# Kernel tuning notes

Hardware: AMD Instinct MI355X
Metric: run time of the kernel (lower is better)

Reference implementation:

```python
import jax, jax.numpy as jnp
import numpy as np

N_NODES = 100000
N_EDGES = 1600000
IN_FEATS = 256
OUT_FEATS = 128


def setup_inputs() -> dict:
    key = jax.random.key(0)
    k1, k2, k3, k4 = jax.random.split(key, 4)
    feat = jax.random.normal(k1, (N_NODES, IN_FEATS), dtype=jnp.float32)
    src = jax.random.randint(k2, (N_EDGES,), 0, N_NODES, dtype=jnp.int64)
    dst = jax.random.randint(k3, (N_EDGES,), 0, N_NODES, dtype=jnp.int64)
    W = jax.random.normal(k4, (IN_FEATS, OUT_FEATS), dtype=jnp.float32) * (1.0 / np.sqrt(IN_FEATS))
    b = jnp.zeros((OUT_FEATS,), dtype=jnp.float32)
    return {"feat": feat, "src": src, "dst": dst, "W": W, "b": b}


def reference(feat, src, dst, W, b):
    # norm = 'both': symmetric degree normalization, clip degrees at 1
    ones = jnp.ones((src.shape[0],), dtype=jnp.float32)
    out_deg = jax.ops.segment_sum(ones, src, num_segments=N_NODES)  # out-degree per src node
    in_deg = jax.ops.segment_sum(ones, dst, num_segments=N_NODES)   # in-degree per dst node
    norm_src = jnp.power(jnp.clip(out_deg, 1.0, None), -0.5)[:, None]  # (N,1)
    norm_dst = jnp.power(jnp.clip(in_deg, 1.0, None), -0.5)[:, None]   # (N,1)

    h = feat * norm_src
    # in_feats (256) > out_feats (128): apply W before aggregation
    h = h @ W  # (N, out_feats)
    # copy_src + sum aggregation over edges (SpMM)
    msgs = h[src]  # (E, out_feats)
    rst = jax.ops.segment_sum(msgs, dst, num_segments=N_NODES)  # (N, out_feats)
    rst = rst * norm_dst
    rst = rst + b
    return rst
```

## Files before the change

### kernel.cpp

```cpp
#include <hip/hip_runtime.h>
#include <hip/hip_bf16.h>
#include <cstddef>

#define NN 100000
#define NE 1600000
#define INF 256
#define OUTF 128
#define NBKT 196
#define BSH 9
#define P1B 250
#define EPB 6400
#define SCL (NBKT * P1B)
#define SCLP 49152

typedef __bf16 bf16x8 __attribute__((ext_vector_type(8)));
typedef float f32x4 __attribute__((ext_vector_type(4)));

__device__ __forceinline__ float bflo(uint v) { return __uint_as_float(v << 16); }
__device__ __forceinline__ float bfhi(uint v) { return __uint_as_float(v & 0xffff0000u); }

__device__ __forceinline__ void gload16(const void* g, void* l) {
  __builtin_amdgcn_global_load_lds((const __attribute__((address_space(1))) void*)g,
                                   (__attribute__((address_space(3))) void*)l, 16, 0, 0);
}

__global__ __launch_bounds__(256) void k_p1a(const int* __restrict__ src,
                                             const int* __restrict__ dst,
                                             int* __restrict__ ghd,
                                             int* __restrict__ ghs,
                                             const float* __restrict__ W,
                                             __bf16* __restrict__ Wt) {
  if (blockIdx.x >= P1B) {
    int i = (blockIdx.x - P1B) * 256 + threadIdx.x;
    if (i < SCLP - SCL) { ghd[SCL + i] = 0; ghs[SCL + i] = 0; }
    int n = i & 127, k = i >> 7;
    Wt[n * INF + k] = (__bf16)W[k * OUTF + n];
    return;
  }
  __shared__ int lhd[NBKT], lhs[NBKT];
  const int t = threadIdx.x;
  if (t < NBKT) { lhd[t] = 0; lhs[t] = 0; }
  __syncthreads();
  const int base = blockIdx.x * EPB;
#pragma unroll
  for (int i = 0; i < EPB / 256; ++i) {
    int e = base + i * 256 + t;
    atomicAdd(&lhd[dst[e] >> BSH], 1);
    atomicAdd(&lhs[src[e] >> BSH], 1);
  }
  __syncthreads();
  if (t < NBKT) {
    ghd[t * P1B + blockIdx.x] = lhd[t];
    ghs[t * P1B + blockIdx.x] = lhs[t];
  }
}

__global__ __launch_bounds__(1024) void k_p1b(int* __restrict__ ghd,
                                              int* __restrict__ ghs,
                                              int* __restrict__ row_start) {
  int* a = blockIdx.x ? ghs : ghd;
  __shared__ int wsum[16];
  const int t = threadIdx.x;
  const int lane = t & 63, wid = t >> 6;
  int4 v[12];
  const int4* p = (const int4*)(a + t * 48);
#pragma unroll
  for (int i = 0; i < 12; ++i) v[i] = p[i];
  int s = 0;
#pragma unroll
  for (int i = 0; i < 12; ++i) s += v[i].x + v[i].y + v[i].z + v[i].w;
  const int mysum = s;
#pragma unroll
  for (int d = 1; d < 64; d <<= 1) {
    int u = __shfl_up(s, d);
    if (lane >= d) s += u;
  }
  if (lane == 63) wsum[wid] = s;
  __syncthreads();
  if (wid == 0) {
    int ws = (lane < 16) ? wsum[lane] : 0;
    int inc = ws;
#pragma unroll
    for (int d = 1; d < 16; d <<= 1) {
      int u = __shfl_up(inc, d);
      if (lane >= d) inc += u;
    }
    if (lane < 16) wsum[lane] = inc - ws;
  }
  __syncthreads();
  int ex = wsum[wid] + s - mysum;
#pragma unroll
  for (int i = 0; i < 12; ++i) {
    int4 w;
    w.x = ex; ex += v[i].x;
    w.y = ex; ex += v[i].y;
    w.z = ex; ex += v[i].z;
    w.w = ex; ex += v[i].w;
    ((int4*)(a + t * 48))[i] = w;
  }
  if (blockIdx.x == 0 && t == 0) row_start[NN] = NE;
}

__global__ __launch_bounds__(256) void k_p1c(const int* __restrict__ src,
                                             const int* __restrict__ dst,
                                             const int* __restrict__ ghd,
                                             const int* __restrict__ ghs,
                                             uint* __restrict__ rec_d,
                                             ushort* __restrict__ rec_s) {
  __shared__ int od[NBKT], os[NBKT];
  const int t = threadIdx.x;
  if (t < NBKT) {
    od[t] = ghd[t * P1B + blockIdx.x];
    os[t] = ghs[t * P1B + blockIdx.x];
  }
  __syncthreads();
  const int base = blockIdx.x * EPB;
#pragma unroll
  for (int i = 0; i < EPB / 256; ++i) {
    int e = base + i * 256 + t;
    int s = src[e], d = dst[e];
    int p = atomicAdd(&od[d >> BSH], 1);
    rec_d[p] = ((uint)s << BSH) | (uint)(d & 511);
    int q = atomicAdd(&os[s >> BSH], 1);
    rec_s[q] = (ushort)(s & 511);
  }
}

__global__ __launch_bounds__(256) void k_p2(const int* __restrict__ ghd,
                                            const int* __restrict__ ghs,
                                            const uint* __restrict__ rec_d,
                                            const ushort* __restrict__ rec_s,
                                            int* __restrict__ edge_src,
                                            int* __restrict__ row_start,
                                            float* __restrict__ ns) {
  __shared__ int lh[512];
  __shared__ int sc[256];
  const int k = blockIdx.x, t = threadIdx.x;
  {
    const int base = ghd[k * P1B];
    const int end = (k == NBKT - 1) ? NE : ghd[(k + 1) * P1B];
    lh[t] = 0; lh[t + 256] = 0;
    __syncthreads();
    for (int j = base + t; j < end; j += 256) atomicAdd(&lh[rec_d[j] & 511], 1);
    __syncthreads();
    int a0 = lh[2 * t], a1 = lh[2 * t + 1];
    sc[t] = a0 + a1;
    __syncthreads();
    for (int off = 1; off < 256; off <<= 1) {
      int add = (t >= off) ? sc[t - off] : 0;
      __syncthreads();
      sc[t] += add;
      __syncthreads();
    }
    int ex = t ? sc[t - 1] : 0;
    int e0 = ex, e1 = ex + a0;
    int n0 = k * 512 + 2 * t;
    if (n0 < NN) row_start[n0] = base + e0;
    if (n0 + 1 < NN) row_start[n0 + 1] = base + e1;
    __syncthreads();
    lh[2 * t] = base + e0;
    lh[2 * t + 1] = base + e1;
    __syncthreads();
    for (int j = base + t; j < end; j += 256) {
      uint r = rec_d[j];
      int p = atomicAdd(&lh[r & 511], 1);
      edge_src[p] = (int)(r >> BSH);
    }
  }
  __syncthreads();
  {
    const int base = ghs[k * P1B];
    const int end = (k == NBKT - 1) ? NE : ghs[(k + 1) * P1B];
    lh[t] = 0; lh[t + 256] = 0;
    __syncthreads();
    for (int j = base + t; j < end; j += 256) atomicAdd(&lh[rec_s[j]], 1);
    __syncthreads();
    int n0 = k * 512 + t, n1 = n0 + 256;
    if (n0 < NN) { int c = lh[t];       ns[n0] = rsqrtf((float)(c > 1 ? c : 1)); }
    if (n1 < NN) { int c = lh[t + 256]; ns[n1] = rsqrtf((float)(c > 1 ? c : 1)); }
  }
}

__global__ __launch_bounds__(256, 2) void k_gemm(const float* __restrict__ feat,
                                                 const __bf16* __restrict__ Wt,
                                                 __bf16* __restrict__ h) {
  __shared__ float lA[2][128 * 64];
  const int tid = threadIdx.x;
  const int w = tid >> 6, l = tid & 63;
  const int lr = l & 15, lg = l >> 4;
  const int bm = blockIdx.x * 128;

#define STAGE(b, t)                                                            \
  {                                                                            \
    _Pragma("unroll")                                                          \
    for (int i = 0; i < 8; ++i) {                                              \
      int chunk = i * 256 + tid;                                               \
      int row = chunk >> 4, cp = chunk & 15;                                   \
      int gr = bm + row; if (gr >= NN) gr = NN - 1;                            \
      int sc = cp ^ (row & 7);                                                 \
      gload16(feat + (size_t)gr * INF + (t) * 64 + sc * 4,                     \
              &lA[b][0] + (size_t)chunk * 4);                                  \
    }                                                                          \
  }

  STAGE(0, 0);

  f32x4 acc[2][8];
#pragma unroll
  for (int i = 0; i < 2; ++i)
#pragma unroll
    for (int j = 0; j < 8; ++j) acc[i][j] = (f32x4)0.0f;

  __syncthreads();

  for (int t = 0; t < 4; ++t) {
    if (t < 3) STAGE((t + 1) & 1, t + 1);
    const float* lb = &lA[t & 1][0];
    const __bf16* bp = Wt + (size_t)lr * INF + t * 64 + lg * 8;
    bf16x8 bfrag[2][8];
#pragma unroll
    for (int kk = 0; kk < 2; ++kk)
#pragma unroll
      for (int nf = 0; nf < 8; ++nf)
        bfrag[kk][nf] = *(const bf16x8*)(bp + (size_t)nf * 16 * INF + kk * 32);
#pragma unroll
    for (int kk = 0; kk < 2; ++kk) {
#pragma unroll
      for (int mf = 0; mf < 2; ++mf) {
        int row = w * 32 + mf * 16 + lr;
        int c = kk * 8 + lg * 2;
        f32x4 x0 = *(const f32x4*)(lb + row * 64 + ((c ^ (row & 7)) << 2));
        f32x4 x1 = *(const f32x4*)(lb + row * 64 + (((c + 1) ^ (row & 7)) << 2));
        bf16x8 a;
#pragma unroll
        for (int j = 0; j < 4; ++j) {
          a[j] = (__bf16)x0[j];
          a[4 + j] = (__bf16)x1[j];
        }
#pragma unroll
        for (int nf = 0; nf < 8; ++nf)
          acc[mf][nf] = __builtin_amdgcn_mfma_f32_16x16x32_bf16(a, bfrag[kk][nf], acc[mf][nf], 0, 0, 0);
      }
    }
    __syncthreads();
  }

#pragma unroll
  for (int mf = 0; mf < 2; ++mf) {
#pragma unroll
    for (int r = 0; r < 4; ++r) {
      int row = bm + w * 32 + mf * 16 + lg * 4 + r;
      if (row < NN) {
        __bf16* hp = h + (size_t)row * OUTF + lr;
#pragma unroll
        for (int nf = 0; nf < 8; ++nf)
          hp[nf * 16] = (__bf16)(acc[mf][nf][r]);
      }
    }
  }
#undef STAGE
}

__global__ __launch_bounds__(256) void k_aggr(const uint4* __restrict__ h4,
                                              const int* __restrict__ row_start,
                                              const float* __restrict__ ns,
                                              const int* __restrict__ edge_src,
                                              const float* __restrict__ bias,
                                              float* __restrict__ out) {
  const int wave = threadIdx.x >> 6;
  const int lane = threadIdx.x & 63;
  const int q = lane >> 4;
  const int cl = lane & 15;
  const int n = blockIdx.x * 4 + wave;
  const int s0 = row_start[n];
  const int s1 = row_start[n + 1];
  const int cnt = s1 - s0;

  float a0 = 0.f, a1 = 0.f, a2 = 0.f, a3 = 0.f, a4 = 0.f, a5 = 0.f, a6 = 0.f, a7 = 0.f;
  for (int j0 = 0; j0 < cnt; j0 += 64) {
    int nb = cnt - j0; if (nb > 64) nb = 64;
    int idv = 0; float nsv = 0.f;
    if (lane < nb) idv = edge_src[s0 + j0 + lane];
    if (lane < nb) nsv = ns[idv];
#pragma unroll 4
    for (int j = 0; j < nb; j += 4) {
      int jj = j + q;
      int e = __shfl(idv, jj);
      float w = __shfl(nsv, jj);
      if (jj < nb) {
        uint4 v = h4[(size_t)e * 16 + cl];
        a0 += w * bflo(v.x); a1 += w * bfhi(v.x);
        a2 += w * bflo(v.y); a3 += w * bfhi(v.y);
        a4 += w * bflo(v.z); a5 += w * bfhi(v.z);
        a6 += w * bflo(v.w); a7 += w * bfhi(v.w);
      }
    }
  }
  a0 += __shfl_xor(a0, 16); a1 += __shfl_xor(a1, 16); a2 += __shfl_xor(a2, 16); a3 += __shfl_xor(a3, 16);
  a4 += __shfl_xor(a4, 16); a5 += __shfl_xor(a5, 16); a6 += __shfl_xor(a6, 16); a7 += __shfl_xor(a7, 16);
  a0 += __shfl_xor(a0, 32); a1 += __shfl_xor(a1, 32); a2 += __shfl_xor(a2, 32); a3 += __shfl_xor(a3, 32);
  a4 += __shfl_xor(a4, 32); a5 += __shfl_xor(a5, 32); a6 += __shfl_xor(a6, 32); a7 += __shfl_xor(a7, 32);

  if (q == 0) {
    float ndv = rsqrtf((float)(cnt > 1 ? cnt : 1));
    const float4* b4 = (const float4*)bias;
    float4 ba = b4[2 * cl], bb = b4[2 * cl + 1];
    float4 o0, o1;
    o0.x = a0 * ndv + ba.x; o0.y = a1 * ndv + ba.y; o0.z = a2 * ndv + ba.z; o0.w = a3 * ndv + ba.w;
    o1.x = a4 * ndv + bb.x; o1.y = a5 * ndv + bb.y; o1.z = a6 * ndv + bb.z; o1.w = a7 * ndv + bb.w;
    float4* op = (float4*)(out + (size_t)n * OUTF);
    op[2 * cl] = o0;
    op[2 * cl + 1] = o1;
  }
}

extern "C" void kernel_launch(void* const* d_in, const int* in_sizes, int n_in,
                              void* d_out, int out_size, void* d_ws, size_t ws_size,
                              hipStream_t stream) {
  const float* feat = (const float*)d_in[0];
  const int* src = (const int*)d_in[1];
  const int* dst = (const int*)d_in[2];
  const float* Wm = (const float*)d_in[3];
  const float* bias = (const float*)d_in[4];
  float* out = (float*)d_out;

  char* ws = (char*)d_ws;
  __bf16* h        = (__bf16*)(ws + 0);
  __bf16* Wt       = (__bf16*)(ws + 25600000);
  int*    ghd      = (int*)(ws + 25665536);
  int*    ghs      = (int*)(ws + 25862144);
  uint*   rec_d    = (uint*)(ws + 26058752);
  ushort* rec_s    = (ushort*)(ws + 32458752);
  int*    edge_src = (int*)(ws + 35658752);
  int*    row_start= (int*)(ws + 42058752);
  float*  ns       = (float*)(ws + 42458768);

  k_p1a<<<P1B + 128, 256, 0, stream>>>(src, dst, ghd, ghs, Wm, Wt);
  k_p1b<<<2, 1024, 0, stream>>>(ghd, ghs, row_start);
  k_p1c<<<P1B, 256, 0, stream>>>(src, dst, ghd, ghs, rec_d, rec_s);
  k_p2<<<NBKT, 256, 0, stream>>>(ghd, ghs, rec_d, rec_s, edge_src, row_start, ns);
  k_gemm<<<(NN + 127) / 128, 256, 0, stream>>>(feat, Wt, h);
  k_aggr<<<NN / 4, 256, 0, stream>>>((const uint4*)h, row_start, ns, edge_src, bias, out);
}
```

Baseline: 186.2 us.

## Slice h by feature columns per XCD and fold source norm into GEMM

```diff
diff --git a/kernel.cpp b/kernel.cpp
--- a/kernel.cpp
+++ b/kernel.cpp
@@ -17,7 +17,6 @@
 typedef float f32x4 __attribute__((ext_vector_type(4)));
 
 __device__ __forceinline__ float bflo(uint v) { return __uint_as_float(v << 16); }
-__device__ __forceinline__ float bfhi(uint v) { return __uint_as_float(v & 0xffff0000u); }
 
 __device__ __forceinline__ void gload16(const void* g, void* l) {
   __builtin_amdgcn_global_load_lds((const __attribute__((address_space(1))) void*)g,
@@ -183,6 +182,7 @@
 
 __global__ __launch_bounds__(256, 2) void k_gemm(const float* __restrict__ feat,
                                                  const __bf16* __restrict__ Wt,
+                                                 const float* __restrict__ ns,
                                                  __bf16* __restrict__ h) {
   __shared__ float lA[2][128 * 64];
   const int tid = threadIdx.x;
@@ -251,66 +251,42 @@
     for (int r = 0; r < 4; ++r) {
       int row = bm + w * 32 + mf * 16 + lg * 4 + r;
       if (row < NN) {
-        __bf16* hp = h + (size_t)row * OUTF + lr;
+        float nsv = ns[row];
 #pragma unroll
         for (int nf = 0; nf < 8; ++nf)
-          hp[nf * 16] = (__bf16)(acc[mf][nf][r]);
+          h[((size_t)nf * NN + row) * 16 + lr] = (__bf16)(acc[mf][nf][r] * nsv);
       }
     }
   }
 #undef STAGE
 }
 
-__global__ __launch_bounds__(256) void k_aggr(const uint4* __restrict__ h4,
+__global__ __launch_bounds__(256) void k_aggr(const ushort* __restrict__ hsl,
                                               const int* __restrict__ row_start,
-                                              const float* __restrict__ ns,
                                               const int* __restrict__ edge_src,
                                               const float* __restrict__ bias,
                                               float* __restrict__ out) {
-  const int wave = threadIdx.x >> 6;
-  const int lane = threadIdx.x & 63;
-  const int q = lane >> 4;
-  const int cl = lane & 15;
-  const int n = blockIdx.x * 4 + wave;
-  const int s0 = row_start[n];
-  const int s1 = row_start[n + 1];
-  const int cnt = s1 - s0;
-
-  float a0 = 0.f, a1 = 0.f, a2 = 0.f, a3 = 0.f, a4 = 0.f, a5 = 0.f, a6 = 0.f, a7 = 0.f;
-  for (int j0 = 0; j0 < cnt; j0 += 64) {
-    int nb = cnt - j0; if (nb > 64) nb = 64;
-    int idv = 0; float nsv = 0.f;
-    if (lane < nb) idv = edge_src[s0 + j0 + lane];
-    if (lane < nb) nsv = ns[idv];
+  const int slice = blockIdx.x & 7;
+  const int chunk = blockIdx.x >> 3;
+  const int strip = threadIdx.x >> 4;
+  const int cl = threadIdx.x & 15;
+  const ushort* hs = hsl + (size_t)slice * NN * 16 + cl;
+  const float bv = bias[slice * 16 + cl];
+  const int n0 = chunk * 512 + strip * 32;
+
+  for (int i = 0; i < 32; ++i) {
+    int n = n0 + i;
+    if (n >= NN) return;
+    int s0 = row_start[n], s1 = row_start[n + 1];
+    float acc = 0.f;
 #pragma unroll 4
-    for (int j = 0; j < nb; j += 4) {
-      int jj = j + q;
-      int e = __shfl(idv, jj);
-      float w = __shfl(nsv, jj);
-      if (jj < nb) {
-        uint4 v = h4[(size_t)e * 16 + cl];
-        a0 += w * bflo(v.x); a1 += w * bfhi(v.x);
-        a2 += w * bflo(v.y); a3 += w * bfhi(v.y);
-        a4 += w * bflo(v.z); a5 += w * bfhi(v.z);
-        a6 += w * bflo(v.w); a7 += w * bfhi(v.w);
-      }
-    }
-  }
-  a0 += __shfl_xor(a0, 16); a1 += __shfl_xor(a1, 16); a2 += __shfl_xor(a2, 16); a3 += __shfl_xor(a3, 16);
-  a4 += __shfl_xor(a4, 16); a5 += __shfl_xor(a5, 16); a6 += __shfl_xor(a6, 16); a7 += __shfl_xor(a7, 16);
-  a0 += __shfl_xor(a0, 32); a1 += __shfl_xor(a1, 32); a2 += __shfl_xor(a2, 32); a3 += __shfl_xor(a3, 32);
-  a4 += __shfl_xor(a4, 32); a5 += __shfl_xor(a5, 32); a6 += __shfl_xor(a6, 32); a7 += __shfl_xor(a7, 32);
-
-  if (q == 0) {
+    for (int j = s0; j < s1; ++j) {
+      int e = edge_src[j];
+      acc += bflo((uint)hs[(size_t)e * 16]);
+    }
+    int cnt = s1 - s0;
     float ndv = rsqrtf((float)(cnt > 1 ? cnt : 1));
-    const float4* b4 = (const float4*)bias;
-    float4 ba = b4[2 * cl], bb = b4[2 * cl + 1];
-    float4 o0, o1;
-    o0.x = a0 * ndv + ba.x; o0.y = a1 * ndv + ba.y; o0.z = a2 * ndv + ba.z; o0.w = a3 * ndv + ba.w;
-    o1.x = a4 * ndv + bb.x; o1.y = a5 * ndv + bb.y; o1.z = a6 * ndv + bb.z; o1.w = a7 * ndv + bb.w;
-    float4* op = (float4*)(out + (size_t)n * OUTF);
-    op[2 * cl] = o0;
-    op[2 * cl + 1] = o1;
+    out[(size_t)n * OUTF + slice * 16 + cl] = acc * ndv + bv;
   }
 }
 
@@ -339,6 +315,6 @@
   k_p1b<<<2, 1024, 0, stream>>>(ghd, ghs, row_start);
   k_p1c<<<P1B, 256, 0, stream>>>(src, dst, ghd, ghs, rec_d, rec_s);
   k_p2<<<NBKT, 256, 0, stream>>>(ghd, ghs, rec_d, rec_s, edge_src, row_start, ns);
-  k_gemm<<<(NN + 127) / 128, 256, 0, stream>>>(feat, Wt, h);
-  k_aggr<<<NN / 4, 256, 0, stream>>>((const uint4*)h, row_start, ns, edge_src, bias, out);
-}
+  k_gemm<<<(NN + 127) / 128, 256, 0, stream>>>(feat, Wt, ns, h);
+  k_aggr<<<196 * 8, 256, 0, stream>>>((const ushort*)h, row_start, edge_src, bias, out);
+}
```

New measurement: 294.3 us. +58.0%, slower.
